# Kernel tuning notes

Measured on AMD Instinct MI355X. Metric: run time of the kernel, lower is better.

Reference implementation:

```python
import jax, jax.numpy as jnp
import numpy as np

BN_EPS = 1e-3  # keras BatchNormalization default


def setup_inputs() -> dict:
    key = jax.random.key(0)
    ks = jax.random.split(key, 8)
    B, T, H, W, C = 2, 8, 28, 28, 256
    Ci = 128
    s_in = 1.0 / np.sqrt(C)
    s_ci = 1.0 / np.sqrt(Ci)
    return {
        "x": jax.random.normal(ks[0], (B, T, H, W, C), dtype=jnp.float32),
        "Wg": jax.random.normal(ks[1], (C, Ci), dtype=jnp.float32) * s_in,
        "bg": jnp.zeros((Ci,), dtype=jnp.float32),
        "Wt": jax.random.normal(ks[2], (C, Ci), dtype=jnp.float32) * s_in,
        "bt": jnp.zeros((Ci,), dtype=jnp.float32),
        "Wp": jax.random.normal(ks[3], (C, Ci), dtype=jnp.float32) * s_in,
        "bp": jnp.zeros((Ci,), dtype=jnp.float32),
        "Wo": jax.random.normal(ks[4], (Ci, C), dtype=jnp.float32) * s_ci,
        "bo": jnp.zeros((C,), dtype=jnp.float32),
        "gamma": jnp.ones((C,), dtype=jnp.float32),
        "beta": jnp.zeros((C,), dtype=jnp.float32),
        "moving_mean": jnp.zeros((C,), dtype=jnp.float32),
        "moving_var": jnp.ones((C,), dtype=jnp.float32),
    }


def reference(x, Wg, bg, Wt, bt, Wp, bp, Wo, bo, gamma, beta, moving_mean, moving_var):
    B, T, H, W, C = x.shape
    Ci = Wg.shape[1]
    N = T * H * W
    xf = x.reshape(B, N, C)  # flatten spatial-temporal positions
    # 1x1x1 convs are per-position channel GEMMs
    g_x = xf @ Wg + bg        # [B, N, Ci]
    theta_x = xf @ Wt + bt    # [B, N, Ci]
    phi_x = xf @ Wp + bp      # [B, N, Ci]
    # f = softmax(theta @ phi^T) -- unscaled single-head global attention
    f = jnp.einsum('bnc,bmc->bnm', theta_x, phi_x)  # [B, N, N]
    f = jax.nn.softmax(f, axis=-1)
    y = jnp.einsum('bnm,bmc->bnc', f, g_x)           # [B, N, Ci]
    # conv_out (1x1x1) back to C channels
    y = y @ Wo + bo                                   # [B, N, C]
    # BatchNorm, inference mode (training=None -> moving statistics)
    y = gamma * (y - moving_mean) * jax.lax.rsqrt(moving_var + BN_EPS) + beta
    return x + y.reshape(B, T, H, W, C)
```

## Files before the change

### kernel.cpp

```cpp
#include <hip/hip_runtime.h>

#define BB 2
#define NN 6272
#define CC 256
#define CI 128
#define SEG 7
#define KVSEG (NN / SEG)
#define NIT (KVSEG / 32)
#define LOG2E 1.44269504088896f
#define THR 12.0f

typedef _Float16 f16;
typedef __attribute__((ext_vector_type(2))) __fp16 fp16v2;
typedef __attribute__((ext_vector_type(8))) _Float16 f16x8;
typedef __attribute__((ext_vector_type(4))) float f32x4;

__global__ __launch_bounds__(256) void prep_kernel(
    const float* __restrict__ Wg, const float* __restrict__ Wt, const float* __restrict__ Wp,
    const float* __restrict__ Wo, const float* __restrict__ bg, const float* __restrict__ bt,
    const float* __restrict__ bp, const float* __restrict__ bo,
    const float* __restrict__ gamma, const float* __restrict__ beta,
    const float* __restrict__ mmean, const float* __restrict__ mvar,
    f16* __restrict__ WallT, f16* __restrict__ WoT,
    float* __restrict__ ball, float* __restrict__ bnsc, float* __restrict__ bnsh)
{
    const int idx = blockIdx.x * 256 + threadIdx.x;
    if (idx < 384*256) {
        const int j = idx >> 8, k = idx & 255;
        float v;
        if (j < 128)      v = Wg[k*CI + j];
        else if (j < 256) v = Wt[k*CI + (j-128)] * LOG2E;
        else              v = Wp[k*CI + (j-256)];
        WallT[j*256 + k] = (f16)v;
    } else if (idx < 384*256 + 256*128) {
        const int i2 = idx - 384*256;
        const int ci = i2 >> 7, k = i2 & 127;
        WoT[ci*CI + k] = (f16)Wo[k*CC + ci];
    } else {
        const int i3 = idx - (384*256 + 256*128);
        if (i3 < 384) {
            float v;
            if (i3 < 128)      v = bg[i3];
            else if (i3 < 256) v = bt[i3-128] * LOG2E;
            else               v = bp[i3-256];
            ball[i3] = v;
        } else if (i3 < 640) {
            const int c = i3 - 384;
            bnsc[c] = gamma[c] * rsqrtf(mvar[c] + 1e-3f);
        } else if (i3 < 896) {
            const int c = i3 - 640;
            float sc = gamma[c] * rsqrtf(mvar[c] + 1e-3f);
            bnsh[c] = beta[c] + sc * (bo[c] - mmean[c]);
        }
    }
}

__global__ __launch_bounds__(256) void proj_gemm(
    const float* __restrict__ x, const f16* __restrict__ WallT, const float* __restrict__ ball,
    f16* __restrict__ th, f16* __restrict__ ph, f16* __restrict__ gT)
{
    __shared__ __align__(16) f16 xls[16*264];
    __shared__ __align__(16) f16 gls[128*24];

    const int tid = threadIdx.x;
    const int wid = tid >> 6, lane = tid & 63;
    const int l15 = lane & 15, lg = lane >> 4;
    const int p0 = blockIdx.x * 16;
    const int nq = wid;

    {
        const int row = tid >> 4, seg = (tid & 15) * 16;
        const float* xsrc = x + (size_t)(p0 + row) * CC + seg;
        f16 buf[16];
        #pragma unroll
        for (int i = 0; i < 4; ++i) {
            float4 v = *reinterpret_cast<const float4*>(xsrc + 4*i);
            buf[4*i+0]=(f16)v.x; buf[4*i+1]=(f16)v.y; buf[4*i+2]=(f16)v.z; buf[4*i+3]=(f16)v.w;
        }
        *reinterpret_cast<f16x8*>(&xls[row*264 + seg])     = *reinterpret_cast<f16x8*>(&buf[0]);
        *reinterpret_cast<f16x8*>(&xls[row*264 + seg + 8]) = *reinterpret_cast<f16x8*>(&buf[8]);
    }
    __syncthreads();

    f32x4 acc[6];
    #pragma unroll
    for (int t = 0; t < 6; ++t) acc[t] = (f32x4){0.f,0.f,0.f,0.f};

    const f16* wbase = WallT + (size_t)(nq*96 + l15)*256 + lg*8;
    for (int kk = 0; kk < 8; ++kk) {
        f16x8 a = *reinterpret_cast<const f16x8*>(&xls[l15*264 + kk*32 + lg*8]);
        #pragma unroll
        for (int t = 0; t < 6; ++t) {
            f16x8 bfr = *reinterpret_cast<const f16x8*>(wbase + (size_t)t*16*256 + kk*32);
            acc[t] = __builtin_amdgcn_mfma_f32_16x16x32_f16(a, bfr, acc[t], 0, 0, 0);
        }
    }

    const int bidx = (p0 >= NN) ? 1 : 0;
    const int n0 = p0 - bidx * NN;
    const int prow = lg * 4;

    #pragma unroll
    for (int t = 0; t < 6; ++t) {
        const int j0 = nq*96 + t*16;
        const float bv = ball[j0 + l15];
        if (j0 < 128) {
            #pragma unroll
            for (int r = 0; r < 4; ++r)
                gls[(j0 + l15)*24 + prow + r] = (f16)(acc[t][r] + bv);
        } else if (j0 < 256) {
            f16* dst = th + (size_t)(p0 + prow)*CI + (j0 - 128) + l15;
            #pragma unroll
            for (int r = 0; r < 4; ++r)
                dst[(size_t)r*CI] = (f16)(acc[t][r] + bv);
        } else {
            f16* dst = ph + (size_t)(p0 + prow)*CI + (j0 - 256) + l15;
            #pragma unroll
            for (int r = 0; r < 4; ++r)
                dst[(size_t)r*CI] = (f16)(acc[t][r] + bv);
        }
    }
    __syncthreads();
    {
        const int ci = tid >> 1, part = tid & 1;
        f16x8 v = *reinterpret_cast<const f16x8*>(&gls[ci*24 + part*8]);
        f16* gdst = gT + ((size_t)bidx*(NN/32) + (n0 >> 5))*(CI*32)
                       + ci*32 + (n0 & 16) + part*8;
        *reinterpret_cast<f16x8*>(gdst) = v;
    }
}

__global__ __launch_bounds__(256, 3) void attn_kernel(
    const f16* __restrict__ th, const f16* __restrict__ ph,
    const f16* __restrict__ gT, float* __restrict__ pacc, float* __restrict__ pml)
{
    __shared__ __align__(16) f16 ph_lds[2][32 * 128];
    __shared__ __align__(16) f16 g_lds[2][128 * 32];
    __shared__ __align__(16) f16 pT_lds[4][2][16][40];

    const int b   = blockIdx.z;
    const int seg = blockIdx.y;
    const int tid = threadIdx.x;
    const int wid = tid >> 6;
    const int lane = tid & 63;
    const int l15 = lane & 15;
    const int lg  = lane >> 4;
    const int qw  = blockIdx.x * 128 + wid * 32;

    const f16* thb = th + (size_t)b * NN * CI;
    const f16* phb = ph + (size_t)b * NN * CI;
    const f16* gTb = gT + (size_t)b * (NN/32) * (CI*32);

    f16x8 bf[2][4];
    #pragma unroll
    for (int qt = 0; qt < 2; ++qt) {
        const f16* trow = thb + (size_t)(qw + qt*16 + l15) * CI + lg * 8;
        #pragma unroll
        for (int kk = 0; kk < 4; ++kk)
            bf[qt][kk] = *reinterpret_cast<const f16x8*>(trow + kk * 32);
    }

    f32x4 acc[2][8];
    f32x4 accl[2];
    float m[2] = {-INFINITY, -INFINITY};
    #pragma unroll
    for (int qt = 0; qt < 2; ++qt) {
        #pragma unroll
        for (int ct = 0; ct < 8; ++ct) acc[qt][ct] = (f32x4){0.f,0.f,0.f,0.f};
        accl[qt] = (f32x4){0.f,0.f,0.f,0.f};
    }

    const f16x8 onesA = {(f16)1,(f16)1,(f16)1,(f16)1,(f16)1,(f16)1,(f16)1,(f16)1};

    const int prow = tid >> 3, pcol = (tid & 7) * 16;
    const int pswz = (prow & 7) << 3;
    const int pc0 = pcol ^ pswz, pc1 = (pcol + 8) ^ pswz;
    const int grow = tid >> 1, gcs = (tid & 1) * 16;
    const int gswz = ((grow >> 1) & 3) << 3;
    const int gc0 = gcs ^ gswz, gc1 = (gcs + 8) ^ gswz;

    const int kv_base = seg * KVSEG;
    const int t0 = kv_base >> 5;

    {
        const f16* ps = phb + (size_t)(kv_base + prow) * CI + pcol;
        f16x8 a = *reinterpret_cast<const f16x8*>(ps);
        f16x8 c = *reinterpret_cast<const f16x8*>(ps + 8);
        const f16* gs = gTb + (size_t)t0 * (CI*32) + tid * 16;
        f16x8 g0 = *reinterpret_cast<const f16x8*>(gs);
        f16x8 g1 = *reinterpret_cast<const f16x8*>(gs + 8);
        *reinterpret_cast<f16x8*>(&ph_lds[0][prow*128 + pc0]) = a;
        *reinterpret_cast<f16x8*>(&ph_lds[0][prow*128 + pc1]) = c;
        *reinterpret_cast<f16x8*>(&g_lds[0][grow*32 + gc0])   = g0;
        *reinterpret_cast<f16x8*>(&g_lds[0][grow*32 + gc1])   = g1;
    }
    __syncthreads();

    #pragma unroll 1
    for (int it = 0; it < NIT; ++it) {
        const int cur = it & 1, nxt = cur ^ 1;
        const bool havenext = (it + 1 < NIT);
        const int itn = havenext ? (it + 1) : it;

        const f16* ps = phb + (size_t)(kv_base + itn*32 + prow) * CI + pcol;
        f16x8 pv0 = *reinterpret_cast<const f16x8*>(ps);
        f16x8 pv1 = *reinterpret_cast<const f16x8*>(ps + 8);
        const f16* gs = gTb + (size_t)(t0 + itn) * (CI*32) + tid * 16;
        f16x8 gv0 = *reinterpret_cast<const f16x8*>(gs);
        f16x8 gv1 = *reinterpret_cast<const f16x8*>(gs + 8);

        const f16* cb = &ph_lds[cur][0];
        f32x4 s00 = (f32x4){0.f,0.f,0.f,0.f}, s01 = (f32x4){0.f,0.f,0.f,0.f};
        f32x4 s10 = (f32x4){0.f,0.f,0.f,0.f}, s11 = (f32x4){0.f,0.f,0.f,0.f};
        const int xsw = (l15 & 7) << 3;
        #pragma unroll
        for (int kk = 0; kk < 4; ++kk) {
            const int coff = (kk*32 + lg*8) ^ xsw;
            f16x8 a0 = *reinterpret_cast<const f16x8*>(&cb[l15*128 + coff]);
            f16x8 a1 = *reinterpret_cast<const f16x8*>(&cb[(16 + l15)*128 + coff]);
            s00 = __builtin_amdgcn_mfma_f32_16x16x32_f16(a0, bf[0][kk], s00, 0, 0, 0);
            s01 = __builtin_amdgcn_mfma_f32_16x16x32_f16(a1, bf[0][kk], s01, 0, 0, 0);
            s10 = __builtin_amdgcn_mfma_f32_16x16x32_f16(a0, bf[1][kk], s10, 0, 0, 0);
            s11 = __builtin_amdgcn_mfma_f32_16x16x32_f16(a1, bf[1][kk], s11, 0, 0, 0);
        }

        float tm0 = fmaxf(fmaxf(fmaxf(s00[0], s00[1]), fmaxf(s00[2], s00[3])),
                          fmaxf(fmaxf(s01[0], s01[1]), fmaxf(s01[2], s01[3])));
        float tm1 = fmaxf(fmaxf(fmaxf(s10[0], s10[1]), fmaxf(s10[2], s10[3])),
                          fmaxf(fmaxf(s11[0], s11[1]), fmaxf(s11[2], s11[3])));
        tm0 = fmaxf(tm0, __shfl_xor(tm0, 16));
        tm0 = fmaxf(tm0, __shfl_xor(tm0, 32));
        tm1 = fmaxf(tm1, __shfl_xor(tm1, 16));
        tm1 = fmaxf(tm1, __shfl_xor(tm1, 32));
        if (__any((tm0 > m[0] + THR) || (tm1 > m[1] + THR))) {
            float nm0 = fmaxf(m[0], tm0), nm1 = fmaxf(m[1], tm1);
            float sc0 = __builtin_amdgcn_exp2f(m[0] - nm0);
            float sc1 = __builtin_amdgcn_exp2f(m[1] - nm1);
            m[0] = nm0; m[1] = nm1;
            #pragma unroll
            for (int ct = 0; ct < 8; ++ct) {
                acc[0][ct][0] *= sc0; acc[0][ct][1] *= sc0; acc[0][ct][2] *= sc0; acc[0][ct][3] *= sc0;
                acc[1][ct][0] *= sc1; acc[1][ct][1] *= sc1; acc[1][ct][2] *= sc1; acc[1][ct][3] *= sc1;
            }
            accl[0][0] *= sc0; accl[0][1] *= sc0; accl[0][2] *= sc0; accl[0][3] *= sc0;
            accl[1][0] *= sc1; accl[1][1] *= sc1; accl[1][2] *= sc1; accl[1][3] *= sc1;
        }

        {
            union { fp16v2 h[2]; float2 f; } u0, u1;
            u0.h[0] = __builtin_amdgcn_cvt_pkrtz(__builtin_amdgcn_exp2f(s00[0] - m[0]),
                                                 __builtin_amdgcn_exp2f(s00[1] - m[0]));
            u0.h[1] = __builtin_amdgcn_cvt_pkrtz(__builtin_amdgcn_exp2f(s00[2] - m[0]),
                                                 __builtin_amdgcn_exp2f(s00[3] - m[0]));
            u1.h[0] = __builtin_amdgcn_cvt_pkrtz(__builtin_amdgcn_exp2f(s01[0] - m[0]),
                                                 __builtin_amdgcn_exp2f(s01[1] - m[0]));
            u1.h[1] = __builtin_amdgcn_cvt_pkrtz(__builtin_amdgcn_exp2f(s01[2] - m[0]),
                                                 __builtin_amdgcn_exp2f(s01[3] - m[0]));
            *reinterpret_cast<float2*>(&pT_lds[wid][0][l15][4*lg])      = u0.f;
            *reinterpret_cast<float2*>(&pT_lds[wid][0][l15][16 + 4*lg]) = u1.f;
            u0.h[0] = __builtin_amdgcn_cvt_pkrtz(__builtin_amdgcn_exp2f(s10[0] - m[1]),
                                                 __builtin_amdgcn_exp2f(s10[1] - m[1]));
            u0.h[1] = __builtin_amdgcn_cvt_pkrtz(__builtin_amdgcn_exp2f(s10[2] - m[1]),
                                                 __builtin_amdgcn_exp2f(s10[3] - m[1]));
            u1.h[0] = __builtin_amdgcn_cvt_pkrtz(__builtin_amdgcn_exp2f(s11[0] - m[1]),
                                                 __builtin_amdgcn_exp2f(s11[1] - m[1]));
            u1.h[1] = __builtin_amdgcn_cvt_pkrtz(__builtin_amdgcn_exp2f(s11[2] - m[1]),
                                                 __builtin_amdgcn_exp2f(s11[3] - m[1]));
            *reinterpret_cast<float2*>(&pT_lds[wid][1][l15][4*lg])      = u0.f;
            *reinterpret_cast<float2*>(&pT_lds[wid][1][l15][16 + 4*lg]) = u1.f;
        }
        asm volatile("s_waitcnt lgkmcnt(0)" ::: "memory");
        f16x8 pa0 = *reinterpret_cast<const f16x8*>(&pT_lds[wid][0][l15][8*lg]);
        f16x8 pa1 = *reinterpret_cast<const f16x8*>(&pT_lds[wid][1][l15][8*lg]);

        const f16* gb = &g_lds[cur][0];
        const int grsw = ((l15 >> 1) & 3) << 3;
        #pragma unroll
        for (int ct = 0; ct < 8; ++ct) {
            f16x8 ga = *reinterpret_cast<const f16x8*>(&gb[(ct*16 + l15)*32 + (lg*8 ^ grsw)]);
            acc[0][ct] = __builtin_amdgcn_mfma_f32_16x16x32_f16(ga, pa0, acc[0][ct], 0, 0, 0);
            acc[1][ct] = __builtin_amdgcn_mfma_f32_16x16x32_f16(ga, pa1, acc[1][ct], 0, 0, 0);
        }
        accl[0] = __builtin_amdgcn_mfma_f32_16x16x32_f16(onesA, pa0, accl[0], 0, 0, 0);
        accl[1] = __builtin_amdgcn_mfma_f32_16x16x32_f16(onesA, pa1, accl[1], 0, 0, 0);

        if (havenext) {
            *reinterpret_cast<f16x8*>(&ph_lds[nxt][prow*128 + pc0]) = pv0;
            *reinterpret_cast<f16x8*>(&ph_lds[nxt][prow*128 + pc1]) = pv1;
            *reinterpret_cast<f16x8*>(&g_lds[nxt][grow*32 + gc0])   = gv0;
            *reinterpret_cast<f16x8*>(&g_lds[nxt][grow*32 + gc1])   = gv1;
        }
        __syncthreads();
    }

    #pragma unroll
    for (int qt = 0; qt < 2; ++qt) {
        float* pb = pacc + (size_t)(b*SEG + seg) * CI * NN + qw + qt*16 + l15;
        #pragma unroll
        for (int ct = 0; ct < 8; ++ct)
            #pragma unroll
            for (int r = 0; r < 4; ++r)
                pb[(size_t)(ct*16 + lg*4 + r) * NN] = acc[qt][ct][r];
    }

    if (lg == 0) {
        #pragma unroll
        for (int qt = 0; qt < 2; ++qt) {
            float* mlb = pml + ((size_t)(b*SEG + seg) * NN + qw + qt*16 + l15) * 2;
            mlb[0] = m[qt];
            mlb[1] = accl[qt][0];
        }
    }
}

__global__ __launch_bounds__(256) void combine_kernel(
    const float* __restrict__ pacc, const float* __restrict__ pml,
    f16* __restrict__ yh)
{
    const int qL = threadIdx.x & 31;
    const int cg = threadIdx.x >> 5;
    const int q  = blockIdx.x * 32 + qL;
    const int b  = blockIdx.y;

    float mv[SEG], lv[SEG];
    #pragma unroll
    for (int s = 0; s < SEG; ++s) {
        const float* p = pml + ((size_t)(b*SEG + s) * NN + q) * 2;
        mv[s] = p[0];
        lv[s] = p[1];
    }
    float M = mv[0];
    #pragma unroll
    for (int s = 1; s < SEG; ++s) M = fmaxf(M, mv[s]);
    float wsum = 0.f, w[SEG];
    #pragma unroll
    for (int s = 0; s < SEG; ++s) {
        w[s] = __builtin_amdgcn_exp2f(mv[s] - M);
        wsum = fmaf(w[s], lv[s], wsum);
    }
    const float inv = 1.0f / wsum;

    const int c0 = cg * 16;
    float o[16];
    #pragma unroll
    for (int i = 0; i < 16; ++i) o[i] = 0.f;
    for (int s = 0; s < SEG; ++s) {
        const float* pb = pacc + ((size_t)(b*SEG + s) * CI + c0) * NN + q;
        #pragma unroll
        for (int i = 0; i < 16; ++i)
            o[i] = fmaf(w[s], pb[(size_t)i * NN], o[i]);
    }
    f16 oh[16];
    #pragma unroll
    for (int i = 0; i < 16; ++i) oh[i] = (f16)(o[i] * inv);
    f16* yo = yh + ((size_t)b * NN + q) * CI + c0;
    *reinterpret_cast<f16x8*>(yo)     = *reinterpret_cast<f16x8*>(&oh[0]);
    *reinterpret_cast<f16x8*>(yo + 8) = *reinterpret_cast<f16x8*>(&oh[8]);
}

__global__ __launch_bounds__(256) void out_gemm(
    const float* __restrict__ x, const f16* __restrict__ yh, const f16* __restrict__ WoT,
    const float* __restrict__ bnsc, const float* __restrict__ bnsh, float* __restrict__ out)
{
    const int tid = threadIdx.x;
    const int wid = tid >> 6, lane = tid & 63;
    const int l15 = lane & 15, lg = lane >> 4;
    const int p0 = blockIdx.x * 16;
    const int nq = wid;

    f32x4 acc[4];
    #pragma unroll
    for (int t = 0; t < 4; ++t) acc[t] = (f32x4){0.f,0.f,0.f,0.f};

    const f16* ya = yh + (size_t)(p0 + l15)*CI + lg*8;
    const f16* wb = WoT + (size_t)(nq*64 + l15)*CI + lg*8;
    #pragma unroll
    for (int kk = 0; kk < 4; ++kk) {
        f16x8 a = *reinterpret_cast<const f16x8*>(ya + kk*32);
        #pragma unroll
        for (int t = 0; t < 4; ++t) {
            f16x8 bfr = *reinterpret_cast<const f16x8*>(wb + (size_t)t*16*CI + kk*32);
            acc[t] = __builtin_amdgcn_mfma_f32_16x16x32_f16(a, bfr, acc[t], 0, 0, 0);
        }
    }

    #pragma unroll
    for (int t = 0; t < 4; ++t) {
        const int ci = nq*64 + t*16 + l15;
        const float sc = bnsc[ci], sh = bnsh[ci];
        #pragma unroll
        for (int r = 0; r < 4; ++r) {
            const size_t idx = (size_t)(p0 + lg*4 + r)*CC + ci;
            out[idx] = x[idx] + fmaf(sc, acc[t][r], sh);
        }
    }
}

extern "C" void kernel_launch(void* const* d_in, const int* in_sizes, int n_in,
                              void* d_out, int out_size, void* d_ws, size_t ws_size,
                              hipStream_t stream)
{
    const float* x     = (const float*)d_in[0];
    const float* Wg    = (const float*)d_in[1];
    const float* bg    = (const float*)d_in[2];
    const float* Wt    = (const float*)d_in[3];
    const float* bt    = (const float*)d_in[4];
    const float* Wp    = (const float*)d_in[5];
    const float* bp    = (const float*)d_in[6];
    const float* Wo    = (const float*)d_in[7];
    const float* bo    = (const float*)d_in[8];
    const float* gamma = (const float*)d_in[9];
    const float* beta  = (const float*)d_in[10];
    const float* mmean = (const float*)d_in[11];
    const float* mvar  = (const float*)d_in[12];
    float* out = (float*)d_out;

    const size_t PB = (size_t)BB * NN * CI;
    f16*   th   = (f16*)d_ws;
    f16*   ph   = th + PB;
    f16*   gT   = ph + PB;
    float* pacc = (float*)(gT + PB);
    float* pml  = pacc + (size_t)BB * SEG * NN * CI;
    f16*   yh   = (f16*)(pml + (size_t)BB * SEG * NN * 2);
    f16*   WallT= yh + PB;
    f16*   WoT  = WallT + 384*256;
    float* ball = (float*)(WoT + 256*CI);
    float* bnsc = ball + 384;
    float* bnsh = bnsc + 256;

    prep_kernel<<<516, 256, 0, stream>>>(Wg, Wt, Wp, Wo, bg, bt, bp, bo,
                                         gamma, beta, mmean, mvar,
                                         WallT, WoT, ball, bnsc, bnsh);
    proj_gemm<<<BB * NN / 16, 256, 0, stream>>>(x, WallT, ball, th, ph, gT);
    attn_kernel<<<dim3(NN / 128, SEG, BB), 256, 0, stream>>>(th, ph, gT, pacc, pml);
    combine_kernel<<<dim3(NN / 32, BB), 256, 0, stream>>>(pacc, pml, yh);
    out_gemm<<<BB * NN / 16, 256, 0, stream>>>(x, yh, WoT, bnsc, bnsh, out);
}
```

Before: 116.7 us.

## Software-pipeline QK^T one tile ahead and prefetch KV two iterations ahead

Restructures the flash-attention loop so the score MFMAs for the next KV tile are issued while the current tile's softmax and PV MFMAs run, with global loads prefetched two iterations ahead into the double buffer. It also drops an explicit lgkmcnt wait. The aim is to hide exp and LDS latency behind MFMA work. In exchange it holds more registers for the extra score accumulators and now needs two barriers per iteration, which may lower occupancy and add sync cost.

```diff
diff --git a/kernel.cpp b/kernel.cpp
--- a/kernel.cpp
+++ b/kernel.cpp
@@ -181,6 +181,7 @@
 
     const int kv_base = seg * KVSEG;
     const int t0 = kv_base >> 5;
+    const int xsw = (l15 & 7) << 3;
 
     {
         const f16* ps = phb + (size_t)(kv_base + prow) * CI + pcol;
@@ -196,32 +197,61 @@
     }
     __syncthreads();
 
-    #pragma unroll 1
-    for (int it = 0; it < NIT; ++it) {
-        const int cur = it & 1, nxt = cur ^ 1;
-        const bool havenext = (it + 1 < NIT);
-        const int itn = havenext ? (it + 1) : it;
-
-        const f16* ps = phb + (size_t)(kv_base + itn*32 + prow) * CI + pcol;
+    f32x4 s00, s01, s10, s11;
+    {
+        const f16* ps = phb + (size_t)(kv_base + 32 + prow) * CI + pcol;
         f16x8 pv0 = *reinterpret_cast<const f16x8*>(ps);
         f16x8 pv1 = *reinterpret_cast<const f16x8*>(ps + 8);
-        const f16* gs = gTb + (size_t)(t0 + itn) * (CI*32) + tid * 16;
+        const f16* gs = gTb + (size_t)(t0 + 1) * (CI*32) + tid * 16;
         f16x8 gv0 = *reinterpret_cast<const f16x8*>(gs);
         f16x8 gv1 = *reinterpret_cast<const f16x8*>(gs + 8);
 
-        const f16* cb = &ph_lds[cur][0];
-        f32x4 s00 = (f32x4){0.f,0.f,0.f,0.f}, s01 = (f32x4){0.f,0.f,0.f,0.f};
-        f32x4 s10 = (f32x4){0.f,0.f,0.f,0.f}, s11 = (f32x4){0.f,0.f,0.f,0.f};
-        const int xsw = (l15 & 7) << 3;
+        s00 = (f32x4){0.f,0.f,0.f,0.f}; s01 = (f32x4){0.f,0.f,0.f,0.f};
+        s10 = (f32x4){0.f,0.f,0.f,0.f}; s11 = (f32x4){0.f,0.f,0.f,0.f};
         #pragma unroll
         for (int kk = 0; kk < 4; ++kk) {
             const int coff = (kk*32 + lg*8) ^ xsw;
-            f16x8 a0 = *reinterpret_cast<const f16x8*>(&cb[l15*128 + coff]);
-            f16x8 a1 = *reinterpret_cast<const f16x8*>(&cb[(16 + l15)*128 + coff]);
+            f16x8 a0 = *reinterpret_cast<const f16x8*>(&ph_lds[0][l15*128 + coff]);
+            f16x8 a1 = *reinterpret_cast<const f16x8*>(&ph_lds[0][(16 + l15)*128 + coff]);
             s00 = __builtin_amdgcn_mfma_f32_16x16x32_f16(a0, bf[0][kk], s00, 0, 0, 0);
             s01 = __builtin_amdgcn_mfma_f32_16x16x32_f16(a1, bf[0][kk], s01, 0, 0, 0);
             s10 = __builtin_amdgcn_mfma_f32_16x16x32_f16(a0, bf[1][kk], s10, 0, 0, 0);
             s11 = __builtin_amdgcn_mfma_f32_16x16x32_f16(a1, bf[1][kk], s11, 0, 0, 0);
+        }
+        *reinterpret_cast<f16x8*>(&ph_lds[1][prow*128 + pc0]) = pv0;
+        *reinterpret_cast<f16x8*>(&ph_lds[1][prow*128 + pc1]) = pv1;
+        *reinterpret_cast<f16x8*>(&g_lds[1][grow*32 + gc0])   = gv0;
+        *reinterpret_cast<f16x8*>(&g_lds[1][grow*32 + gc1])   = gv1;
+    }
+    __syncthreads();
+
+    #pragma unroll 1
+    for (int it = 0; it < NIT; ++it) {
+        const int cur = it & 1, nxt = cur ^ 1;
+        const bool have2 = (it + 2 < NIT);
+        const int it2 = have2 ? (it + 2) : (NIT - 1);
+
+        const f16* ps = phb + (size_t)(kv_base + it2*32 + prow) * CI + pcol;
+        f16x8 pv0 = *reinterpret_cast<const f16x8*>(ps);
+        f16x8 pv1 = *reinterpret_cast<const f16x8*>(ps + 8);
+        const f16* gs = gTb + (size_t)(t0 + it2) * (CI*32) + tid * 16;
+        f16x8 gv0 = *reinterpret_cast<const f16x8*>(gs);
+        f16x8 gv1 = *reinterpret_cast<const f16x8*>(gs + 8);
+
+        f32x4 n00 = (f32x4){0.f,0.f,0.f,0.f}, n01 = (f32x4){0.f,0.f,0.f,0.f};
+        f32x4 n10 = (f32x4){0.f,0.f,0.f,0.f}, n11 = (f32x4){0.f,0.f,0.f,0.f};
+        if (it + 1 < NIT) {
+            const f16* cb = &ph_lds[nxt][0];
+            #pragma unroll
+            for (int kk = 0; kk < 4; ++kk) {
+                const int coff = (kk*32 + lg*8) ^ xsw;
+                f16x8 a0 = *reinterpret_cast<const f16x8*>(&cb[l15*128 + coff]);
+                f16x8 a1 = *reinterpret_cast<const f16x8*>(&cb[(16 + l15)*128 + coff]);
+                n00 = __builtin_amdgcn_mfma_f32_16x16x32_f16(a0, bf[0][kk], n00, 0, 0, 0);
+                n01 = __builtin_amdgcn_mfma_f32_16x16x32_f16(a1, bf[0][kk], n01, 0, 0, 0);
+                n10 = __builtin_amdgcn_mfma_f32_16x16x32_f16(a0, bf[1][kk], n10, 0, 0, 0);
+                n11 = __builtin_amdgcn_mfma_f32_16x16x32_f16(a1, bf[1][kk], n11, 0, 0, 0);
+            }
         }
 
         float tm0 = fmaxf(fmaxf(fmaxf(s00[0], s00[1]), fmaxf(s00[2], s00[3])),
@@ -269,7 +299,6 @@
             *reinterpret_cast<float2*>(&pT_lds[wid][1][l15][4*lg])      = u0.f;
             *reinterpret_cast<float2*>(&pT_lds[wid][1][l15][16 + 4*lg]) = u1.f;
         }
-        asm volatile("s_waitcnt lgkmcnt(0)" ::: "memory");
         f16x8 pa0 = *reinterpret_cast<const f16x8*>(&pT_lds[wid][0][l15][8*lg]);
         f16x8 pa1 = *reinterpret_cast<const f16x8*>(&pT_lds[wid][1][l15][8*lg]);
 
@@ -284,13 +313,16 @@
         accl[0] = __builtin_amdgcn_mfma_f32_16x16x32_f16(onesA, pa0, accl[0], 0, 0, 0);
         accl[1] = __builtin_amdgcn_mfma_f32_16x16x32_f16(onesA, pa1, accl[1], 0, 0, 0);
 
-        if (havenext) {
-            *reinterpret_cast<f16x8*>(&ph_lds[nxt][prow*128 + pc0]) = pv0;
-            *reinterpret_cast<f16x8*>(&ph_lds[nxt][prow*128 + pc1]) = pv1;
-            *reinterpret_cast<f16x8*>(&g_lds[nxt][grow*32 + gc0])   = gv0;
-            *reinterpret_cast<f16x8*>(&g_lds[nxt][grow*32 + gc1])   = gv1;
-        }
-        __syncthreads();
+        if (have2) {
+            __syncthreads();
+            *reinterpret_cast<f16x8*>(&ph_lds[cur][prow*128 + pc0]) = pv0;
+            *reinterpret_cast<f16x8*>(&ph_lds[cur][prow*128 + pc1]) = pv1;
+            *reinterpret_cast<f16x8*>(&g_lds[cur][grow*32 + gc0])   = gv0;
+            *reinterpret_cast<f16x8*>(&g_lds[cur][grow*32 + gc1])   = gv1;
+            __syncthreads();
+        }
+
+        s00 = n00; s01 = n01; s10 = n10; s11 = n11;
     }
 
     #pragma unroll
```

New measurement: 155.7 us. +33.4%, slower.
